# Kernel tuning notes

Measured on AMD Instinct MI355X. Metric: run time of the kernel, lower is better.

The kernel has to match this reference:

```python
import jax, jax.numpy as jnp
import numpy as np

B, S, H = 2, 2048, 2048
NH, NKV, HD = 16, 4, 128
GROUPS = NH // NKV  # 4
ROPE_BASE = 10000.0


def _rope_tables(seq_len, dim):
    inv_freq = 1.0 / (ROPE_BASE ** (jnp.arange(0, dim, 2, dtype=jnp.float32) / dim))
    t = jnp.arange(seq_len, dtype=jnp.float32)
    freqs = jnp.outer(t, inv_freq)            # [S, HD/2]
    emb = jnp.concatenate([freqs, freqs], -1)  # [S, HD]
    return jnp.cos(emb), jnp.sin(emb)


def _rotate_half(x):
    x1, x2 = x[..., : x.shape[-1] // 2], x[..., x.shape[-1] // 2:]
    return jnp.concatenate([-x2, x1], axis=-1)


def setup_inputs() -> dict:
    key = jax.random.key(0)
    ks = jax.random.split(key, 5)
    hidden_states = jax.random.normal(ks[0], (B, S, H), dtype=jnp.float32)
    wq = jax.random.normal(ks[1], (H, NH * HD), dtype=jnp.float32) * 0.02
    wk = jax.random.normal(ks[2], (H, NKV * HD), dtype=jnp.float32) * 0.02
    wv = jax.random.normal(ks[3], (H, NKV * HD), dtype=jnp.float32) * 0.02
    wo = jax.random.normal(ks[4], (NH * HD, H), dtype=jnp.float32) * 0.02
    # additive causal mask [1,1,S,S]
    causal = jnp.tril(jnp.ones((S, S), dtype=bool))
    attention_mask = jnp.where(causal, 0.0, jnp.finfo(jnp.float32).min)[None, None]
    return {"hidden_states": hidden_states, "attention_mask": attention_mask,
            "wq": wq, "wk": wk, "wv": wv, "wo": wo}


def reference(hidden_states, attention_mask, wq, wk, wv, wo):
    b, s, _ = hidden_states.shape
    # projections -> [B, heads, S, HD]
    q = (hidden_states @ wq).reshape(b, s, NH, HD).transpose(0, 2, 1, 3)
    k = (hidden_states @ wk).reshape(b, s, NKV, HD).transpose(0, 2, 1, 3)
    v = (hidden_states @ wv).reshape(b, s, NKV, HD).transpose(0, 2, 1, 3)
    cos, sin = _rope_tables(s, HD)             # [S, HD]
    cos = cos[None, None]; sin = sin[None, None]
    q = q * cos + _rotate_half(q) * sin
    k = k * cos + _rotate_half(k) * sin
    # GQA: repeat kv heads (matches repeat_interleave on dim=1)
    k = jnp.repeat(k, GROUPS, axis=1)
    v = jnp.repeat(v, GROUPS, axis=1)
    scores = jnp.einsum("bhqd,bhkd->bhqk", q, k) / jnp.sqrt(jnp.float32(HD))
    scores = scores + attention_mask
    probs = jax.nn.softmax(scores.astype(jnp.float32), axis=-1).astype(q.dtype)
    attn = jnp.einsum("bhqk,bhkd->bhqd", probs, v)
    attn = attn.transpose(0, 2, 1, 3).reshape(b, s, NH * HD)
    return attn @ wo
```

## Files before the change

### kernel.cpp

```cpp
#include <hip/hip_runtime.h>

typedef unsigned short u16;
typedef unsigned int u32;
typedef __attribute__((ext_vector_type(8))) __bf16 bf16x8;
typedef __attribute__((ext_vector_type(8))) u16 u16x8;
typedef __attribute__((ext_vector_type(4))) float f32x4;

#define B_ 2
#define S_ 2048
#define H_ 2048
#define NH_ 16
#define NKV_ 4
#define HD_ 128
#define QSCALE 0.1275179064f

__device__ __forceinline__ u16 f2bf(float f) {
  return __builtin_bit_cast(u16, static_cast<__bf16>(f));
}
__device__ __forceinline__ float bf2f(u16 v) {
  return __builtin_bit_cast(float, (u32)v << 16);
}
__device__ __forceinline__ void gl2lds16(const void* g, void* l) {
  __builtin_amdgcn_global_load_lds((const __attribute__((address_space(1))) u32*)g,
                                   (__attribute__((address_space(3))) u32*)l, 16, 0, 0);
}
__device__ __forceinline__ f32x4 mfma16(bf16x8 a, bf16x8 b, f32x4 c) {
  return __builtin_amdgcn_mfma_f32_16x16x32_bf16(a, b, c, 0, 0, 0);
}

__global__ __launch_bounds__(256) void prologue(const float* __restrict__ hid,
                                                const float* __restrict__ wq,
                                                const float* __restrict__ wk,
                                                const float* __restrict__ wv,
                                                u16* __restrict__ hb,
                                                u16* __restrict__ wqkvT) {
  const int bid = blockIdx.x;
  if (bid < 4096) {
    size_t i = ((size_t)bid * 256 + threadIdx.x) * 8;
    const float4* p = (const float4*)(hid + i);
    float4 a = p[0], b = p[1];
    u16x8 o;
    o[0] = f2bf(a.x); o[1] = f2bf(a.y); o[2] = f2bf(a.z); o[3] = f2bf(a.w);
    o[4] = f2bf(b.x); o[5] = f2bf(b.y); o[6] = f2bf(b.z); o[7] = f2bf(b.w);
    *(u16x8*)(hb + i) = o;
  } else {
    __shared__ float tl[32][33];
    int t = bid - 4096;
    int bx = t % 96, by = t / 96;
    int tx = threadIdx.x & 31, ty = threadIdx.x >> 5;
    int orow0 = bx * 32;
    const float* src;
    int scol0, C;
    if (orow0 < 2048)      { src = wq; scol0 = orow0;        C = 2048; }
    else if (orow0 < 2560) { src = wk; scol0 = orow0 - 2048; C = 512; }
    else                   { src = wv; scol0 = orow0 - 2560; C = 512; }
#pragma unroll
    for (int i = 0; i < 32; i += 8)
      tl[ty + i][tx] = src[(size_t)(by * 32 + ty + i) * C + scol0 + tx];
    __syncthreads();
#pragma unroll
    for (int i = 0; i < 32; i += 8)
      wqkvT[(size_t)(orow0 + ty + i) * 2048 + by * 32 + tx] = f2bf(tl[tx][ty + i]);
  }
}

__global__ __launch_bounds__(256) void midpass(u16* __restrict__ kvb,
                                               u16* __restrict__ vt,
                                               float* __restrict__ tab) {
  const int bid = blockIdx.x;
  if (bid < 512) {
    int idx = bid * 256 + threadIdx.x;
    int s = idx >> 6, i = idx & 63;
    float inv = exp2f((float)i * -0.20762050593045702f);
    float ang = (float)s * inv;
    tab[2 * idx] = cosf(ang);
    tab[2 * idx + 1] = sinf(ang);
  } else if (bid < 1024) {
    int idx = (bid - 512) * 256 + threadIdx.x;
    int grp = idx & 7;
    int h = (idx >> 3) & 3;
    int tok = idx >> 5;
    int s = tok & (S_ - 1);
    u16* p = kvb + (size_t)tok * 1024 + (h << 7) + grp * 8;
    u16x8 lo = *(u16x8*)p;
    u16x8 hi = *(u16x8*)(p + 64);
    u16x8 olo, ohi;
#pragma unroll
    for (int j = 0; j < 8; j++) {
      int i = grp * 8 + j;
      float inv = exp2f((float)i * -0.20762050593045702f);
      float ang = (float)s * inv;
      float c = cosf(ang), sn = sinf(ang);
      float xl = bf2f(lo[j]), xh = bf2f(hi[j]);
      olo[j] = f2bf(xl * c - xh * sn);
      ohi[j] = f2bf(xh * c + xl * sn);
    }
    *(u16x8*)p = olo;
    *(u16x8*)(p + 64) = ohi;
  } else {
    __shared__ u16 tl[32][33];
    int t = bid - 1024;
    int sx = t & 63, dx = (t >> 6) & 15, b = t >> 10;
    int tx = threadIdx.x & 31, ty = threadIdx.x >> 5;
#pragma unroll
    for (int i = 0; i < 32; i += 8)
      tl[ty + i][tx] = kvb[(size_t)(b * S_ + sx * 32 + ty + i) * 1024 + 512 + dx * 32 + tx];
    __syncthreads();
#pragma unroll
    for (int i = 0; i < 32; i += 8)
      vt[(size_t)(b * 512 + dx * 32 + ty + i) * 2048 + sx * 32 + tx] = tl[tx][ty + i];
  }
}

__global__ __launch_bounds__(256) void transpose_f32_bf16(const float* __restrict__ in,
                                                          u16* __restrict__ out,
                                                          int R, int C) {
  __shared__ float tl[32][33];
  int bx = blockIdx.x, by = blockIdx.y;
  int tx = threadIdx.x & 31, ty = threadIdx.x >> 5;
#pragma unroll
  for (int i = 0; i < 32; i += 8)
    tl[ty + i][tx] = in[(size_t)(by * 32 + ty + i) * C + bx * 32 + tx];
  __syncthreads();
#pragma unroll
  for (int i = 0; i < 32; i += 8)
    out[(size_t)(bx * 32 + ty + i) * R + by * 32 + tx] = f2bf(tl[tx][ty + i]);
}

__global__ __launch_bounds__(256) void gemm_bt1(const u16* __restrict__ A,
                                                const u16* __restrict__ BT,
                                                u16* __restrict__ Qb,
                                                u16* __restrict__ KVb,
                                                int M, int N, int K) {
  __shared__ u16 As[2 * 128 * 32];
  __shared__ u16 Bs[2 * 128 * 32];
  const int Mt = M >> 7;
  const int nwg = gridDim.x;
  int wg = (blockIdx.x & 7) * (nwg >> 3) + (blockIdx.x >> 3);
  int tm = wg % Mt, tn = wg / Mt;
  const size_t m0 = (size_t)tm << 7, n0 = (size_t)tn << 7;
  const int tid = threadIdx.x;
  const int w = tid >> 6, lane = tid & 63;
  const int g = lane >> 4, l15 = lane & 15;
  const int wr = w >> 1, wc = w & 1;

  const int r0 = tid >> 2, s0 = tid & 3;
  const int r1 = (tid + 256) >> 2, s1 = (tid + 256) & 3;
  const u16* Ar0 = A + (m0 + r0) * K + s0 * 8;
  const u16* Ar1 = A + (m0 + r1) * K + s1 * 8;
  const u16* Br0 = BT + (n0 + r0) * K + s0 * 8;
  const u16* Br1 = BT + (n0 + r1) * K + s1 * 8;

  const f32x4 Z4 = {0.f, 0.f, 0.f, 0.f};
  f32x4 acc[4][4];
#pragma unroll
  for (int m = 0; m < 4; m++)
#pragma unroll
    for (int n = 0; n < 4; n++) acc[m][n] = Z4;

  gl2lds16(Ar0, &As[w * 512]);
  gl2lds16(Ar1, &As[w * 512 + 2048]);
  gl2lds16(Br0, &Bs[w * 512]);
  gl2lds16(Br1, &Bs[w * 512 + 2048]);

  const int nk = K >> 5;
  int cur = 0;
  for (int t = 0; t < nk; ++t) {
    if (t + 1 < nk) {
      const int k0 = (t + 1) << 5;
      const int nb = (cur ^ 1) << 12;
      gl2lds16(Ar0 + k0, &As[nb + w * 512]);
      gl2lds16(Ar1 + k0, &As[nb + w * 512 + 2048]);
      gl2lds16(Br0 + k0, &Bs[nb + w * 512]);
      gl2lds16(Br1 + k0, &Bs[nb + w * 512 + 2048]);
      asm volatile("s_waitcnt vmcnt(4)" ::: "memory");
    } else {
      asm volatile("s_waitcnt vmcnt(0)" ::: "memory");
    }
    __builtin_amdgcn_sched_barrier(0);
    __builtin_amdgcn_s_barrier();
    __builtin_amdgcn_sched_barrier(0);
    const int cb = cur << 12;
    bf16x8 af[4], bfr[4];
#pragma unroll
    for (int m = 0; m < 4; m++)
      af[m] = *(const bf16x8*)&As[cb + (wr * 64 + m * 16 + l15) * 32 + g * 8];
#pragma unroll
    for (int n = 0; n < 4; n++)
      bfr[n] = *(const bf16x8*)&Bs[cb + (wc * 64 + n * 16 + l15) * 32 + g * 8];
#pragma unroll
    for (int m = 0; m < 4; m++)
#pragma unroll
      for (int n = 0; n < 4; n++) acc[m][n] = mfma16(af[m], bfr[n], acc[m][n]);
    __builtin_amdgcn_sched_barrier(0);
    __builtin_amdgcn_s_barrier();
    __builtin_amdgcn_sched_barrier(0);
    cur ^= 1;
  }

  u16* C;
  size_t cs, cbase;
  if (n0 < 2048) { C = Qb; cs = 2048; cbase = n0; }
  else           { C = KVb; cs = 1024; cbase = n0 - 2048; }
#pragma unroll
  for (int m = 0; m < 4; m++)
#pragma unroll
    for (int n = 0; n < 4; n++)
#pragma unroll
      for (int r = 0; r < 4; r++) {
        size_t row = m0 + wr * 64 + m * 16 + g * 4 + r;
        C[row * cs + cbase + wc * 64 + n * 16 + l15] = f2bf(acc[m][n][r]);
      }
}

__global__ __launch_bounds__(256) void gemm_o64(const u16* __restrict__ A,
                                                const u16* __restrict__ BT,
                                                float* __restrict__ C) {
  const int K = 2048, N = 2048;
  __shared__ u16 As[2 * 128 * 64];
  __shared__ u16 Bs[2 * 128 * 64];
  const int Mt = 32;
  const int nwg = gridDim.x;
  int wg = (blockIdx.x & 7) * (nwg >> 3) + (blockIdx.x >> 3);
  int tm = wg % Mt, tn = wg / Mt;
  const size_t m0 = (size_t)tm << 7, n0 = (size_t)tn << 7;
  const int tid = threadIdx.x;
  const int w = tid >> 6, lane = tid & 63;
  const int g = lane >> 4, l15 = lane & 15;
  const int wr = w >> 1, wc = w & 1;

  size_t aoff[4], boff[4];
#pragma unroll
  for (int ro = 0; ro < 4; ++ro) {
    int c = ro * 256 + tid;
    int row = c >> 3, seg = c & 7;
    aoff[ro] = (m0 + row) * (size_t)K + 8 * (seg ^ (row & 7));
    boff[ro] = (n0 + row) * (size_t)K + 8 * (seg ^ (row & 7));
  }

  const f32x4 Z4 = {0.f, 0.f, 0.f, 0.f};
  f32x4 acc[4][4];
#pragma unroll
  for (int m = 0; m < 4; m++)
#pragma unroll
    for (int n = 0; n < 4; n++) acc[m][n] = Z4;

#pragma unroll
  for (int ro = 0; ro < 4; ++ro) {
    gl2lds16(A + aoff[ro], &As[ro * 2048 + w * 512]);
    gl2lds16(BT + boff[ro], &Bs[ro * 2048 + w * 512]);
  }

  const int nk = K >> 6;
  int cur = 0;
  for (int t = 0; t < nk; ++t) {
    if (t + 1 < nk) {
      const int k0 = (t + 1) << 6;
      const int nb = (cur ^ 1) << 13;
#pragma unroll
      for (int ro = 0; ro < 4; ++ro) {
        gl2lds16(A + k0 + aoff[ro], &As[nb + ro * 2048 + w * 512]);
        gl2lds16(BT + k0 + boff[ro], &Bs[nb + ro * 2048 + w * 512]);
      }
      asm volatile("s_waitcnt vmcnt(8)" ::: "memory");
    } else {
      asm volatile("s_waitcnt vmcnt(0)" ::: "memory");
    }
    __builtin_amdgcn_sched_barrier(0);
    __builtin_amdgcn_s_barrier();
    __builtin_amdgcn_sched_barrier(0);
    const int cb = cur << 13;
    bf16x8 af[2][4], bfr[2][4];
#pragma unroll
    for (int kk = 0; kk < 2; ++kk) {
#pragma unroll
      for (int m = 0; m < 4; m++)
        af[kk][m] = *(const bf16x8*)&As[cb + (wr * 64 + m * 16 + l15) * 64 +
                                       ((kk * 4 + g) ^ (l15 & 7)) * 8];
#pragma unroll
      for (int n = 0; n < 4; n++)
        bfr[kk][n] = *(const bf16x8*)&Bs[cb + (wc * 64 + n * 16 + l15) * 64 +
                                        ((kk * 4 + g) ^ (l15 & 7)) * 8];
    }
#pragma unroll
    for (int kk = 0; kk < 2; ++kk)
#pragma unroll
      for (int m = 0; m < 4; m++)
#pragma unroll
        for (int n = 0; n < 4; n++)
          acc[m][n] = mfma16(af[kk][m], bfr[kk][n], acc[m][n]);
    __builtin_amdgcn_sched_barrier(0);
    __builtin_amdgcn_s_barrier();
    __builtin_amdgcn_sched_barrier(0);
    cur ^= 1;
  }

#pragma unroll
  for (int m = 0; m < 4; m++)
#pragma unroll
    for (int n = 0; n < 4; n++)
#pragma unroll
      for (int r = 0; r < 4; r++) {
        size_t row = m0 + wr * 64 + m * 16 + g * 4 + r;
        size_t col = n0 + wc * 64 + n * 16 + l15;
        C[row * (size_t)N + col] = acc[m][n][r];
      }
}

__global__ __launch_bounds__(256) void attn_kernel(const u16* __restrict__ Qb,
                                                   const u16* __restrict__ KVb,
                                                   const u16* __restrict__ Vt,
                                                   const float* __restrict__ tab,
                                                   u16* __restrict__ Ob) {
  __shared__ u16 Ks[2][64 * 128];
  __shared__ u16 Vs[2][128 * 64];
  __shared__ u16 Ps[4][16 * 72];
  const int pair = blockIdx.x, h = blockIdx.y, b = blockIdx.z;
  const int kvh = h >> 2;
  const int tid = threadIdx.x, w = tid >> 6, lane = tid & 63;
  const int g = lane >> 4, l15 = lane & 15;
  const f32x4 Z4 = {0.f, 0.f, 0.f, 0.f};
  u16x8 oneu;
#pragma unroll
  for (int j = 0; j < 8; j++) oneu[j] = 0x3f80;
  const bf16x8 ones = __builtin_bit_cast(bf16x8, oneu);

  const u16* Kbase = KVb + (size_t)b * S_ * 1024 + kvh * 128;
  const u16* Vbase = Vt + (size_t)(b * NKV_ + kvh) * HD_ * 2048;

  for (int half = 0; half < 2; ++half) {
    const int qt = half ? pair : 31 - pair;
    const int qrow0 = qt * 64 + w * 16;

    bf16x8 qf[4];
    const u16* qp = Qb + (size_t)(b * S_ + qrow0 + l15) * 2048 + h * 128;
#pragma unroll
    for (int ds = 0; ds < 4; ds++) qf[ds] = *(const bf16x8*)(qp + ds * 32 + g * 8);
    {
      const float2* tq = (const float2*)tab + (size_t)(qrow0 + l15) * 64 + g * 8;
#pragma unroll
      for (int ds = 0; ds < 2; ds++) {
        u16x8 a = __builtin_bit_cast(u16x8, qf[ds]);
        u16x8 bb = __builtin_bit_cast(u16x8, qf[ds + 2]);
#pragma unroll
        for (int j = 0; j < 8; j++) {
          float2 cs = tq[ds * 32 + j];
          float c = cs.x * QSCALE, sn = cs.y * QSCALE;
          float lo = bf2f(a[j]), hi = bf2f(bb[j]);
          a[j] = f2bf(lo * c - hi * sn);
          bb[j] = f2bf(hi * c + lo * sn);
        }
        qf[ds] = __builtin_bit_cast(bf16x8, a);
        qf[ds + 2] = __builtin_bit_cast(bf16x8, bb);
      }
    }

    float m_r[4], l_r[4];
    f32x4 oa[8];
#pragma unroll
    for (int r = 0; r < 4; r++) { m_r[r] = -1e30f; l_r[r] = 0.f; }
#pragma unroll
    for (int n = 0; n < 8; n++) oa[n] = Z4;

    const int nt = qt + 1;
#pragma unroll
    for (int ro = 0; ro < 4; ++ro) {
      int c = ro * 256 + tid;
      int kv = c >> 4, p = c & 15;
      gl2lds16(Kbase + (size_t)kv * 1024 + 8 * (p ^ (kv & 15)), &Ks[0][ro * 2048 + w * 512]);
      int d = c >> 3, p2 = c & 7;
      gl2lds16(Vbase + (size_t)d * 2048 + 8 * (p2 ^ (d & 7)), &Vs[0][ro * 2048 + w * 512]);
    }
    __syncthreads();
    int cur = 0;

    for (int t = 0; t < nt; ++t) {
      const int kv0 = t * 64;
      if (t + 1 < nt) {
        const int nkv0 = kv0 + 64;
#pragma unroll
        for (int ro = 0; ro < 4; ++ro) {
          int c = ro * 256 + tid;
          int kv = c >> 4, p = c & 15;
          gl2lds16(Kbase + (size_t)(nkv0 + kv) * 1024 + 8 * (p ^ (kv & 15)),
                   &Ks[cur ^ 1][ro * 2048 + w * 512]);
          int d = c >> 3, p2 = c & 7;
          gl2lds16(Vbase + (size_t)d * 2048 + nkv0 + 8 * (p2 ^ (d & 7)),
                   &Vs[cur ^ 1][ro * 2048 + w * 512]);
        }
      }

      f32x4 sa[4];
#pragma unroll
      for (int c16 = 0; c16 < 4; c16++) sa[c16] = Z4;
      __builtin_amdgcn_s_setprio(1);
#pragma unroll
      for (int ds = 0; ds < 4; ++ds) {
#pragma unroll
        for (int c16 = 0; c16 < 4; ++c16) {
          bf16x8 kf = *(const bf16x8*)&Ks[cur][(c16 * 16 + l15) * 128 + ((ds * 4 + g) ^ l15) * 8];
          sa[c16] = mfma16(qf[ds], kf, sa[c16]);
        }
      }
      __builtin_amdgcn_s_setprio(0);

      if (kv0 + 63 > qrow0) {
#pragma unroll
        for (int c16 = 0; c16 < 4; c16++)
#pragma unroll
          for (int r = 0; r < 4; r++) {
            if (kv0 + c16 * 16 + l15 > qrow0 + g * 4 + r) sa[c16][r] = -1e30f;
          }
      }

      float lmax[4];
#pragma unroll
      for (int r = 0; r < 4; r++)
        lmax[r] = fmaxf(fmaxf(sa[0][r], sa[1][r]), fmaxf(sa[2][r], sa[3][r]));
      bool need = (lmax[0] > m_r[0] + 11.5415603f) || (lmax[1] > m_r[1] + 11.5415603f) ||
                  (lmax[2] > m_r[2] + 11.5415603f) || (lmax[3] > m_r[3] + 11.5415603f);
      if (__any(need)) {
        float pm[4];
#pragma unroll
        for (int r = 0; r < 4; r++) pm[r] = lmax[r];
#pragma unroll
        for (int off = 1; off < 16; off <<= 1)
#pragma unroll
          for (int r = 0; r < 4; r++) pm[r] = fmaxf(pm[r], __shfl_xor(pm[r], off));
#pragma unroll
        for (int r = 0; r < 4; r++) {
          float mn = fmaxf(m_r[r], pm[r]);
          float corr = exp2f(m_r[r] - mn);
          m_r[r] = mn;
          l_r[r] *= corr;
#pragma unroll
          for (int n = 0; n < 8; n++) oa[n][r] *= corr;
        }
      }

#pragma unroll
      for (int c16 = 0; c16 < 4; c16++)
#pragma unroll
        for (int r = 0; r < 4; r++)
          Ps[w][(g * 4 + r) * 72 + c16 * 16 + l15] =
              f2bf(exp2f(sa[c16][r] - m_r[r]));
      asm volatile("s_waitcnt lgkmcnt(0)" ::: "memory");
      __builtin_amdgcn_sched_barrier(0);

      f32x4 srow = Z4;
      __builtin_amdgcn_s_setprio(1);
#pragma unroll
      for (int ks = 0; ks < 2; ++ks) {
        bf16x8 pa = *(const bf16x8*)&Ps[w][l15 * 72 + ks * 32 + g * 8];
        srow = mfma16(pa, ones, srow);
#pragma unroll
        for (int n = 0; n < 8; n++) {
          bf16x8 vf = *(const bf16x8*)&Vs[cur][(n * 16 + l15) * 64 + (((ks * 4 + g) ^ (l15 & 7))) * 8];
          oa[n] = mfma16(pa, vf, oa[n]);
        }
      }
      __builtin_amdgcn_s_setprio(0);
#pragma unroll
      for (int r = 0; r < 4; r++) l_r[r] += srow[r];

      __syncthreads();
      cur ^= 1;
    }

    float inv[4];
#pragma unroll
    for (int r = 0; r < 4; r++) inv[r] = 1.0f / l_r[r];
#pragma unroll
    for (int n = 0; n < 8; n++)
#pragma unroll
      for (int r = 0; r < 4; r++) {
        size_t row = (size_t)b * S_ + qrow0 + g * 4 + r;
        Ob[row * 2048 + h * 128 + n * 16 + l15] = f2bf(oa[n][r] * inv[r]);
      }
  }
}

extern "C" void kernel_launch(void* const* d_in, const int* in_sizes, int n_in,
                              void* d_out, int out_size, void* d_ws, size_t ws_size,
                              hipStream_t stream) {
  const float* hid = (const float*)d_in[0];
  const float* wq = (const float*)d_in[2];
  const float* wk = (const float*)d_in[3];
  const float* wv = (const float*)d_in[4];
  const float* wo = (const float*)d_in[5];
  float* out = (float*)d_out;
  char* ws = (char*)d_ws;

  u16* hb     = (u16*)(ws);
  u16* wqkvT  = (u16*)(ws + (16u << 20));
  u16* Vt     = (u16*)(ws + (16u << 20));
  float* tab  = (float*)(ws + (20u << 20));
  u16* woT    = (u16*)(ws + (20u << 20));
  u16* Qb     = (u16*)(ws + (28u << 20));
  u16* KVb    = (u16*)(ws + (44u << 20));

  prologue<<<10240, 256, 0, stream>>>(hid, wq, wk, wv, hb, wqkvT);

  gemm_bt1<<<768, 256, 0, stream>>>(hb, wqkvT, Qb, KVb, 4096, 3072, 2048);

  midpass<<<3072, 256, 0, stream>>>(KVb, Vt, tab);

  attn_kernel<<<dim3(16, 16, 2), 256, 0, stream>>>(Qb, KVb, Vt, tab, hb);

  transpose_f32_bf16<<<dim3(64, 64), 256, 0, stream>>>(wo, woT, 2048, 2048);

  gemm_o64<<<512, 256, 0, stream>>>(hb, woT, out);
}
```

Baseline: 220.0 us.

## Fold Wo transpose into midpass and compute Q RoPE inline in attention

Moves the Wo fp32-to-bf16 transpose into the midpass kernel as extra blocks, removing one kernel launch. It also drops the precomputed cos/sin table: the attention kernel now computes the RoPE angles for Q directly with exp2f/cosf/sinf. The workspace layout is reshuffled so woT and Vt no longer alias. This trades a table load for extra transcendental math in the attention prologue, and makes midpass a larger heterogeneous grid.

```diff
diff --git a/kernel.cpp b/kernel.cpp
--- a/kernel.cpp
+++ b/kernel.cpp
@@ -13,6 +13,7 @@
 #define NKV_ 4
 #define HD_ 128
 #define QSCALE 0.1275179064f
+#define NFREQ -0.20762050593045702f
 
 __device__ __forceinline__ u16 f2bf(float f) {
   return __builtin_bit_cast(u16, static_cast<__bf16>(f));
@@ -64,19 +65,24 @@
   }
 }
 
-__global__ __launch_bounds__(256) void midpass(u16* __restrict__ kvb,
-                                               u16* __restrict__ vt,
-                                               float* __restrict__ tab) {
+__global__ __launch_bounds__(256) void midpass(const float* __restrict__ wo,
+                                               u16* __restrict__ kvb,
+                                               u16* __restrict__ woT,
+                                               u16* __restrict__ vt) {
   const int bid = blockIdx.x;
-  if (bid < 512) {
-    int idx = bid * 256 + threadIdx.x;
-    int s = idx >> 6, i = idx & 63;
-    float inv = exp2f((float)i * -0.20762050593045702f);
-    float ang = (float)s * inv;
-    tab[2 * idx] = cosf(ang);
-    tab[2 * idx + 1] = sinf(ang);
-  } else if (bid < 1024) {
-    int idx = (bid - 512) * 256 + threadIdx.x;
+  if (bid < 4096) {
+    __shared__ float tl[32][33];
+    int bx = bid & 63, by = bid >> 6;
+    int tx = threadIdx.x & 31, ty = threadIdx.x >> 5;
+#pragma unroll
+    for (int i = 0; i < 32; i += 8)
+      tl[ty + i][tx] = wo[(size_t)(by * 32 + ty + i) * 2048 + bx * 32 + tx];
+    __syncthreads();
+#pragma unroll
+    for (int i = 0; i < 32; i += 8)
+      woT[(size_t)(bx * 32 + ty + i) * 2048 + by * 32 + tx] = f2bf(tl[tx][ty + i]);
+  } else if (bid < 4608) {
+    int idx = (bid - 4096) * 256 + threadIdx.x;
     int grp = idx & 7;
     int h = (idx >> 3) & 3;
     int tok = idx >> 5;
@@ -88,7 +94,7 @@
 #pragma unroll
     for (int j = 0; j < 8; j++) {
       int i = grp * 8 + j;
-      float inv = exp2f((float)i * -0.20762050593045702f);
+      float inv = exp2f((float)i * NFREQ);
       float ang = (float)s * inv;
       float c = cosf(ang), sn = sinf(ang);
       float xl = bf2f(lo[j]), xh = bf2f(hi[j]);
@@ -99,7 +105,7 @@
     *(u16x8*)(p + 64) = ohi;
   } else {
     __shared__ u16 tl[32][33];
-    int t = bid - 1024;
+    int t = bid - 4608;
     int sx = t & 63, dx = (t >> 6) & 15, b = t >> 10;
     int tx = threadIdx.x & 31, ty = threadIdx.x >> 5;
 #pragma unroll
@@ -110,21 +116,6 @@
     for (int i = 0; i < 32; i += 8)
       vt[(size_t)(b * 512 + dx * 32 + ty + i) * 2048 + sx * 32 + tx] = tl[tx][ty + i];
   }
-}
-
-__global__ __launch_bounds__(256) void transpose_f32_bf16(const float* __restrict__ in,
-                                                          u16* __restrict__ out,
-                                                          int R, int C) {
-  __shared__ float tl[32][33];
-  int bx = blockIdx.x, by = blockIdx.y;
-  int tx = threadIdx.x & 31, ty = threadIdx.x >> 5;
-#pragma unroll
-  for (int i = 0; i < 32; i += 8)
-    tl[ty + i][tx] = in[(size_t)(by * 32 + ty + i) * C + bx * 32 + tx];
-  __syncthreads();
-#pragma unroll
-  for (int i = 0; i < 32; i += 8)
-    out[(size_t)(bx * 32 + ty + i) * R + by * 32 + tx] = f2bf(tl[tx][ty + i]);
 }
 
 __global__ __launch_bounds__(256) void gemm_bt1(const u16* __restrict__ A,
@@ -310,7 +301,6 @@
 __global__ __launch_bounds__(256) void attn_kernel(const u16* __restrict__ Qb,
                                                    const u16* __restrict__ KVb,
                                                    const u16* __restrict__ Vt,
-                                                   const float* __restrict__ tab,
                                                    u16* __restrict__ Ob) {
   __shared__ u16 Ks[2][64 * 128];
   __shared__ u16 Vs[2][128 * 64];
@@ -337,15 +327,17 @@
 #pragma unroll
     for (int ds = 0; ds < 4; ds++) qf[ds] = *(const bf16x8*)(qp + ds * 32 + g * 8);
     {
-      const float2* tq = (const float2*)tab + (size_t)(qrow0 + l15) * 64 + g * 8;
+      const float sf = (float)(qrow0 + l15);
 #pragma unroll
       for (int ds = 0; ds < 2; ds++) {
         u16x8 a = __builtin_bit_cast(u16x8, qf[ds]);
         u16x8 bb = __builtin_bit_cast(u16x8, qf[ds + 2]);
 #pragma unroll
         for (int j = 0; j < 8; j++) {
-          float2 cs = tq[ds * 32 + j];
-          float c = cs.x * QSCALE, sn = cs.y * QSCALE;
+          int i = ds * 32 + g * 8 + j;
+          float inv = exp2f((float)i * NFREQ);
+          float ang = sf * inv;
+          float c = cosf(ang) * QSCALE, sn = sinf(ang) * QSCALE;
           float lo = bf2f(a[j]), hi = bf2f(bb[j]);
           a[j] = f2bf(lo * c - hi * sn);
           bb[j] = f2bf(hi * c + lo * sn);
@@ -493,9 +485,8 @@
 
   u16* hb     = (u16*)(ws);
   u16* wqkvT  = (u16*)(ws + (16u << 20));
-  u16* Vt     = (u16*)(ws + (16u << 20));
-  float* tab  = (float*)(ws + (20u << 20));
-  u16* woT    = (u16*)(ws + (20u << 20));
+  u16* woT    = (u16*)(ws + (16u << 20));
+  u16* Vt     = (u16*)(ws + (24u << 20));
   u16* Qb     = (u16*)(ws + (28u << 20));
   u16* KVb    = (u16*)(ws + (44u << 20));
 
@@ -503,11 +494,9 @@
 
   gemm_bt1<<<768, 256, 0, stream>>>(hb, wqkvT, Qb, KVb, 4096, 3072, 2048);
 
-  midpass<<<3072, 256, 0, stream>>>(KVb, Vt, tab);
-
-  attn_kernel<<<dim3(16, 16, 2), 256, 0, stream>>>(Qb, KVb, Vt, tab, hb);
-
-  transpose_f32_bf16<<<dim3(64, 64), 256, 0, stream>>>(wo, woT, 2048, 2048);
+  midpass<<<6656, 256, 0, stream>>>(wo, KVb, woT, Vt);
+
+  attn_kernel<<<dim3(16, 16, 2), 256, 0, stream>>>(Qb, KVb, Vt, hb);
 
   gemm_o64<<<512, 256, 0, stream>>>(hb, woT, out);
 }
```

Measured after the change: 267.7 us. 21.7% more time.
